# Kernel tuning notes

Measured on AMD Instinct MI355X. Metric: run time of the kernel, lower is better.

The kernel has to match this reference:

```python
import jax, jax.numpy as jnp
import numpy as np

N, E, D, H, K = 8192, 8, 1024, 4096, 2


def setup_inputs() -> dict:
    key = jax.random.key(0)
    ks = jax.random.split(key, 12)
    s = 0.02  # init scale for weights
    return {
        "x": jax.random.normal(ks[0], (N, D), jnp.float32),
        "noise": jax.random.normal(ks[1], (N, E), jnp.float32),
        "Wg_w": jax.random.normal(ks[2], (D, E), jnp.float32) * s,
        "Wg_b": jnp.zeros((E,), jnp.float32),
        "Wn_w": jax.random.normal(ks[3], (D, E), jnp.float32) * s,
        "Wn_b": jnp.zeros((E,), jnp.float32),
        "w1": jax.random.normal(ks[4], (E, D, H), jnp.float32) * s,
        "b1": jnp.zeros((E, H), jnp.float32),
        "w2": jax.random.normal(ks[5], (E, H, D), jnp.float32) * s,
        "b2": jnp.zeros((E, D), jnp.float32),
        "k": K,
    }


def reference(x, noise, Wg_w, Wg_b, Wn_w, Wn_b, w1, b1, w2, b2, k):
    # --- noisy top-k gating: H(x) = Wg(x) + noise * softplus(Wn(x)) ---
    g_logits = x @ Wg_w + Wg_b                       # [N, E]
    n_scale = jax.nn.softplus(x @ Wn_w + Wn_b)       # [N, E]
    h = g_logits + noise * n_scale                   # [N, E]
    topk_vals, topk_inds = jax.lax.top_k(h, k)       # [N, k]
    gates = jax.nn.softmax(topk_vals, axis=-1)       # [N, k]

    # Scatter top-k gates into a dense [N, E] map (zeros for unselected experts),
    # so the weighted combine is exactly sum_j gates[n,j] * expert_{inds[n,j]}(x_n).
    n_tok, n_exp = h.shape
    dense_gates = jnp.zeros((n_tok, n_exp), h.dtype).at[
        jnp.arange(n_tok)[:, None], topk_inds
    ].set(gates)                                     # [N, E]

    # --- per-expert 2-layer MLP: fc2(relu(fc1(x))) ---
    hid = jax.nn.relu(jnp.einsum('nd,edh->neh', x, w1) + b1)  # [N, E, H]
    y = jnp.einsum('neh,ehd->ned', hid, w2) + b2              # [N, E, D]
    out = jnp.einsum('ned,ne->nd', y, dense_gates)            # [N, D]
    return out
```

## Files before the change

### kernel.cpp

```cpp
#include <hip/hip_runtime.h>
#include <hip/hip_bf16.h>

#define NTOK 8192
#define NEXP 8
#define DMODEL 1024
#define DHID 4096

typedef __bf16 bf16x8 __attribute__((ext_vector_type(8)));
typedef float f32x4 __attribute__((ext_vector_type(4)));

__device__ __forceinline__ unsigned short f2bf(float f) {
  return __builtin_bit_cast(unsigned short, __float2bfloat16(f));
}

__device__ __forceinline__ void gload_lds16(const void* g, void* l) {
  __builtin_amdgcn_global_load_lds(
      (const __attribute__((address_space(1))) unsigned int*)g,
      (__attribute__((address_space(3))) unsigned int*)l, 16, 0, 0);
}

__device__ __forceinline__ int imin(int a, int b) { return a < b ? a : b; }

constexpr size_t OFF_XB   = 0;
constexpr size_t OFF_W1T  = OFF_XB + (size_t)NTOK * DMODEL * 2;
constexpr size_t OFF_W2T  = OFF_W1T + (size_t)NEXP * DHID * DMODEL * 2;
constexpr size_t OFF_HID  = OFF_W2T + (size_t)NEXP * DMODEL * DHID * 2;
constexpr size_t OFF_IDX  = OFF_HID + (size_t)NTOK * 2 * DHID * 2;
constexpr size_t OFF_GATE = OFF_IDX + (size_t)NTOK * 2 * 4;
constexpr size_t OFF_LIST = OFF_GATE + (size_t)NTOK * 2 * 4;
constexpr size_t OFF_CNT  = OFF_LIST + (size_t)NTOK * 2 * 4;
constexpr size_t OFF_OFFS = OFF_CNT + 128;
constexpr size_t OFF_CUR  = OFF_OFFS + 128;

__global__ void convert_x_kernel(const float4* __restrict__ in,
                                 ushort4* __restrict__ out, int n4) {
  int i = blockIdx.x * 256 + threadIdx.x;
  if (i < n4) {
    float4 v = in[i];
    ushort4 o;
    o.x = f2bf(v.x); o.y = f2bf(v.y); o.z = f2bf(v.z); o.w = f2bf(v.w);
    out[i] = o;
  }
}

__global__ void transpose_bf16_kernel(const float* __restrict__ in,
                                      unsigned short* __restrict__ out,
                                      int R, int C) {
  __shared__ float sh[32][33];
  const size_t ebase = (size_t)blockIdx.z * R * C;
  const float* ine = in + ebase;
  unsigned short* oute = out + ebase;
  int c0 = blockIdx.x * 32, r0 = blockIdx.y * 32;
  int tx = threadIdx.x & 31, ty = threadIdx.x >> 5;
#pragma unroll
  for (int i = 0; i < 4; ++i) {
    int r = ty + i * 8;
    sh[r][tx] = ine[(size_t)(r0 + r) * C + c0 + tx];
  }
  __syncthreads();
#pragma unroll
  for (int i = 0; i < 4; ++i) {
    int r = ty + i * 8;
    oute[(size_t)(c0 + r) * R + r0 + tx] = f2bf(sh[tx][r]);
  }
}

__global__ void gating_kernel(const float* __restrict__ x,
                              const float* __restrict__ noise,
                              const float* __restrict__ Wg_w,
                              const float* __restrict__ Wg_b,
                              const float* __restrict__ Wn_w,
                              const float* __restrict__ Wn_b,
                              int* __restrict__ topk_idx,
                              float* __restrict__ topk_gate,
                              int* __restrict__ counts) {
  int wave = threadIdx.x >> 6;
  int lane = threadIdx.x & 63;
  int n = blockIdx.x * 4 + wave;
  if (n >= NTOK) return;

  float ag[8] = {0.f, 0.f, 0.f, 0.f, 0.f, 0.f, 0.f, 0.f};
  float an[8] = {0.f, 0.f, 0.f, 0.f, 0.f, 0.f, 0.f, 0.f};
  const float* xr = x + (size_t)n * DMODEL;
#pragma unroll 4
  for (int i = 0; i < DMODEL / 64; ++i) {
    int d = lane + i * 64;
    float xv = xr[d];
    const float4* wg = (const float4*)(Wg_w + (size_t)d * 8);
    const float4* wn = (const float4*)(Wn_w + (size_t)d * 8);
    float4 g0 = wg[0], g1 = wg[1];
    float4 n0 = wn[0], n1 = wn[1];
    ag[0] += xv * g0.x; ag[1] += xv * g0.y; ag[2] += xv * g0.z; ag[3] += xv * g0.w;
    ag[4] += xv * g1.x; ag[5] += xv * g1.y; ag[6] += xv * g1.z; ag[7] += xv * g1.w;
    an[0] += xv * n0.x; an[1] += xv * n0.y; an[2] += xv * n0.z; an[3] += xv * n0.w;
    an[4] += xv * n1.x; an[5] += xv * n1.y; an[6] += xv * n1.z; an[7] += xv * n1.w;
  }
#pragma unroll
  for (int off = 32; off > 0; off >>= 1) {
#pragma unroll
    for (int j = 0; j < 8; ++j) {
      ag[j] += __shfl_down(ag[j], off, 64);
      an[j] += __shfl_down(an[j], off, 64);
    }
  }
  if (lane == 0) {
    float h[8];
#pragma unroll
    for (int e = 0; e < 8; ++e) {
      float gl = ag[e] + Wg_b[e];
      float z = an[e] + Wn_b[e];
      float sp = fmaxf(z, 0.f) + log1pf(expf(-fabsf(z)));
      h[e] = gl + noise[(size_t)n * 8 + e] * sp;
    }
    int i0 = 0; float v0 = h[0];
#pragma unroll
    for (int e = 1; e < 8; ++e)
      if (h[e] > v0) { v0 = h[e]; i0 = e; }
    int i1 = -1; float v1 = -1e30f;
#pragma unroll
    for (int e = 0; e < 8; ++e)
      if (e != i0 && h[e] > v1) { v1 = h[e]; i1 = e; }
    float e1 = expf(v1 - v0);
    float inv = 1.f / (1.f + e1);
    topk_idx[n * 2] = i0;
    topk_idx[n * 2 + 1] = i1;
    topk_gate[n * 2] = inv;
    topk_gate[n * 2 + 1] = e1 * inv;
    atomicAdd(&counts[i0], 1);
    atomicAdd(&counts[i1], 1);
  }
}

__global__ void scan_kernel(const int* __restrict__ counts,
                            int* __restrict__ offsets, int* __restrict__ cursor) {
  if (threadIdx.x == 0) {
    int acc = 0;
    for (int e = 0; e < NEXP; ++e) {
      offsets[e] = acc;
      cursor[e] = acc;
      acc += counts[e];
    }
    offsets[NEXP] = acc;
  }
}

__global__ void scatter_kernel(const int* __restrict__ topk_idx,
                               int* __restrict__ cursor, int* __restrict__ list) {
  int n = blockIdx.x * 256 + threadIdx.x;
  if (n >= NTOK) return;
#pragma unroll
  for (int j = 0; j < 2; ++j) {
    int e = topk_idx[n * 2 + j];
    int pos = atomicAdd(&cursor[e], 1);
    list[pos] = n * 2 + j;
  }
}

template <int MODE>
__global__ __launch_bounds__(256) void expert_gemm(
    const unsigned short* __restrict__ Asrc, const unsigned short* __restrict__ Bt,
    const float* __restrict__ bias, const int* __restrict__ offsets,
    const int* __restrict__ list, const float* __restrict__ gates,
    unsigned short* __restrict__ hid, float* __restrict__ out) {
  constexpr int K = MODE ? DHID : DMODEL;
  constexpr int Nout = MODE ? DMODEL : DHID;

  const int e = blockIdx.z;
  const int off = offsets[e];
  const int ne = offsets[e + 1] - off;
  const int m0 = blockIdx.y * 128;
  if (m0 >= ne) return;
  const int n0 = blockIdx.x * 128;

  __shared__ alignas(16) unsigned short Alds[128 * 32];
  __shared__ alignas(16) unsigned short Blds[128 * 32];

  const int tid = threadIdx.x;
  const int lane = tid & 63;
  const int w = tid >> 6;
  const int wm = (w >> 1) * 64;
  const int wn = (w & 1) * 64;
  const int lr = lane & 15;
  const int kg = lane >> 4;

  const unsigned short* srcA[2];
  const unsigned short* srcB[2];
#pragma unroll
  for (int i = 0; i < 2; ++i) {
    int q = tid + i * 256;
    int r = q >> 2, c = q & 3;
    int p = off + imin(m0 + r, ne - 1);
    if (MODE == 0) {
      int token = list[p] >> 1;
      srcA[i] = Asrc + (size_t)token * DMODEL + c * 8;
    } else {
      srcA[i] = Asrc + (size_t)p * DHID + c * 8;
    }
    srcB[i] = Bt + (size_t)e * Nout * K + (size_t)(n0 + r) * K + c * 8;
  }

  f32x4 acc[4][4] = {};

  for (int kt = 0; kt < K; kt += 32) {
#pragma unroll
    for (int i = 0; i < 2; ++i) {
      int q = tid + i * 256;
      gload_lds16(srcA[i] + kt, &Alds[q * 8]);
      gload_lds16(srcB[i] + kt, &Blds[q * 8]);
    }
    __syncthreads();

    bf16x8 af[4], bfr[4];
#pragma unroll
    for (int mf = 0; mf < 4; ++mf)
      af[mf] = *(const bf16x8*)&Alds[(wm + mf * 16 + lr) * 32 + kg * 8];
#pragma unroll
    for (int nf = 0; nf < 4; ++nf)
      bfr[nf] = *(const bf16x8*)&Blds[(wn + nf * 16 + lr) * 32 + kg * 8];
#pragma unroll
    for (int mf = 0; mf < 4; ++mf)
#pragma unroll
      for (int nf = 0; nf < 4; ++nf)
        acc[mf][nf] = __builtin_amdgcn_mfma_f32_16x16x32_bf16(af[mf], bfr[nf],
                                                              acc[mf][nf], 0, 0, 0);
    __syncthreads();
  }

  if (MODE == 0) {
#pragma unroll
    for (int mf = 0; mf < 4; ++mf) {
#pragma unroll
      for (int i = 0; i < 4; ++i) {
        int rloc = wm + mf * 16 + kg * 4 + i;
        int row = m0 + rloc;
        if (row < ne) {
          size_t p = (size_t)(off + row);
#pragma unroll
          for (int nf = 0; nf < 4; ++nf) {
            int col = n0 + wn + nf * 16 + lr;
            float v = acc[mf][nf][i] + bias[(size_t)e * Nout + col];
            v = fmaxf(v, 0.f);
            hid[p * DHID + col] = f2bf(v);
          }
        }
      }
    }
  } else {
#pragma unroll
    for (int mf = 0; mf < 4; ++mf) {
#pragma unroll
      for (int i = 0; i < 4; ++i) {
        int rloc = wm + mf * 16 + kg * 4 + i;
        int row = m0 + rloc;
        if (row < ne) {
          int lv = list[off + row];
          int token = lv >> 1;
          float g = gates[lv];
#pragma unroll
          for (int nf = 0; nf < 4; ++nf) {
            int col = n0 + wn + nf * 16 + lr;
            float v = (acc[mf][nf][i] + bias[(size_t)e * Nout + col]) * g;
            atomicAdd(&out[(size_t)token * DMODEL + col], v);
          }
        }
      }
    }
  }
}

extern "C" void kernel_launch(void* const* d_in, const int* in_sizes, int n_in,
                              void* d_out, int out_size, void* d_ws, size_t ws_size,
                              hipStream_t stream) {
  const float* x = (const float*)d_in[0];
  const float* noise = (const float*)d_in[1];
  const float* Wg_w = (const float*)d_in[2];
  const float* Wg_b = (const float*)d_in[3];
  const float* Wn_w = (const float*)d_in[4];
  const float* Wn_b = (const float*)d_in[5];
  const float* w1 = (const float*)d_in[6];
  const float* b1 = (const float*)d_in[7];
  const float* w2 = (const float*)d_in[8];
  const float* b2 = (const float*)d_in[9];
  float* out = (float*)d_out;

  char* ws = (char*)d_ws;
  unsigned short* xb = (unsigned short*)(ws + OFF_XB);
  unsigned short* w1t = (unsigned short*)(ws + OFF_W1T);
  unsigned short* w2t = (unsigned short*)(ws + OFF_W2T);
  unsigned short* hid = (unsigned short*)(ws + OFF_HID);
  int* topk_idx = (int*)(ws + OFF_IDX);
  float* topk_gate = (float*)(ws + OFF_GATE);
  int* list = (int*)(ws + OFF_LIST);
  int* counts = (int*)(ws + OFF_CNT);
  int* offsets = (int*)(ws + OFF_OFFS);
  int* cursor = (int*)(ws + OFF_CUR);

  hipMemsetAsync(out, 0, (size_t)NTOK * DMODEL * sizeof(float), stream);
  hipMemsetAsync(counts, 0, NEXP * sizeof(int), stream);

  {
    int n4 = NTOK * DMODEL / 4;
    convert_x_kernel<<<(n4 + 255) / 256, 256, 0, stream>>>((const float4*)x,
                                                           (ushort4*)xb, n4);
  }
  transpose_bf16_kernel<<<dim3(DHID / 32, DMODEL / 32, NEXP), 256, 0, stream>>>(
      w1, w1t, DMODEL, DHID);
  transpose_bf16_kernel<<<dim3(DMODEL / 32, DHID / 32, NEXP), 256, 0, stream>>>(
      w2, w2t, DHID, DMODEL);

  gating_kernel<<<NTOK / 4, 256, 0, stream>>>(x, noise, Wg_w, Wg_b, Wn_w, Wn_b,
                                              topk_idx, topk_gate, counts);
  scan_kernel<<<1, 64, 0, stream>>>(counts, offsets, cursor);
  scatter_kernel<<<NTOK / 256, 256, 0, stream>>>(topk_idx, cursor, list);

  expert_gemm<0><<<dim3(DHID / 128, NTOK / 128, NEXP), 256, 0, stream>>>(
      xb, w1t, b1, offsets, list, topk_gate, hid, nullptr);
  expert_gemm<1><<<dim3(DMODEL / 128, NTOK / 128, NEXP), 256, 0, stream>>>(
      hid, w2t, b2, offsets, list, topk_gate, nullptr, out);
}
```

Baseline: 888.4 us.

## Enlarge expert GEMM tiles to 256x256 with double-buffered swizzled LDS

The expert GEMM grows from 128x128 tiles with 4 waves to 256x256 tiles with 8 waves. It double-buffers the LDS stages so the next k-tile load overlaps the current MFMA work, XOR-swizzles the LDS columns to cut bank conflicts, and remaps block IDs so that adjacent workgroups spread across experts. The weight transpose also moves to 64x64 tiles with float4 loads and ushort4 stores. The aim is more data reuse and latency hiding per block, paid for with higher register and LDS pressure (64KB LDS, 128 accumulator floats per thread) and more wasted rows in the padded tail tiles per expert.

```diff
diff --git a/kernel.cpp b/kernel.cpp
--- a/kernel.cpp
+++ b/kernel.cpp
@@ -46,22 +46,31 @@
 __global__ void transpose_bf16_kernel(const float* __restrict__ in,
                                       unsigned short* __restrict__ out,
                                       int R, int C) {
-  __shared__ float sh[32][33];
+  __shared__ float sh[64][65];
   const size_t ebase = (size_t)blockIdx.z * R * C;
   const float* ine = in + ebase;
   unsigned short* oute = out + ebase;
-  int c0 = blockIdx.x * 32, r0 = blockIdx.y * 32;
-  int tx = threadIdx.x & 31, ty = threadIdx.x >> 5;
-#pragma unroll
-  for (int i = 0; i < 4; ++i) {
-    int r = ty + i * 8;
-    sh[r][tx] = ine[(size_t)(r0 + r) * C + c0 + tx];
+  int c0 = blockIdx.x * 64, r0 = blockIdx.y * 64;
+  int tx = threadIdx.x & 15, ty = threadIdx.x >> 4;
+#pragma unroll
+  for (int p = 0; p < 4; ++p) {
+    int row = ty + p * 16;
+    float4 v = *(const float4*)&ine[(size_t)(r0 + row) * C + c0 + tx * 4];
+    sh[row][tx * 4 + 0] = v.x;
+    sh[row][tx * 4 + 1] = v.y;
+    sh[row][tx * 4 + 2] = v.z;
+    sh[row][tx * 4 + 3] = v.w;
   }
   __syncthreads();
 #pragma unroll
-  for (int i = 0; i < 4; ++i) {
-    int r = ty + i * 8;
-    oute[(size_t)(c0 + r) * R + r0 + tx] = f2bf(sh[tx][r]);
+  for (int p = 0; p < 4; ++p) {
+    int crow = ty + p * 16;
+    ushort4 o;
+    o.x = f2bf(sh[tx * 4 + 0][crow]);
+    o.y = f2bf(sh[tx * 4 + 1][crow]);
+    o.z = f2bf(sh[tx * 4 + 2][crow]);
+    o.w = f2bf(sh[tx * 4 + 3][crow]);
+    *(ushort4*)&oute[(size_t)(c0 + crow) * R + r0 + tx * 4] = o;
   }
 }
 
@@ -157,100 +166,125 @@
 }
 
 template <int MODE>
-__global__ __launch_bounds__(256) void expert_gemm(
+__global__ __launch_bounds__(512, 2) void expert_gemm(
     const unsigned short* __restrict__ Asrc, const unsigned short* __restrict__ Bt,
     const float* __restrict__ bias, const int* __restrict__ offsets,
     const int* __restrict__ list, const float* __restrict__ gates,
     unsigned short* __restrict__ hid, float* __restrict__ out) {
   constexpr int K = MODE ? DHID : DMODEL;
   constexpr int Nout = MODE ? DMODEL : DHID;
-
-  const int e = blockIdx.z;
+  constexpr int NT = K / 32;
+
+  const int gx = gridDim.x, gy = gridDim.y;
+  const int nwg = gx * gy * NEXP;
+  const int lin = blockIdx.x + gx * (blockIdx.y + gy * blockIdx.z);
+  const int wg = (lin & 7) * (nwg >> 3) + (lin >> 3);
+  const int e = wg / (gx * gy);
+  const int t = wg % (gx * gy);
+  const int bx = t / gy;
+  const int by = t % gy;
+
   const int off = offsets[e];
   const int ne = offsets[e + 1] - off;
-  const int m0 = blockIdx.y * 128;
+  const int m0 = by * 256;
   if (m0 >= ne) return;
-  const int n0 = blockIdx.x * 128;
-
-  __shared__ alignas(16) unsigned short Alds[128 * 32];
-  __shared__ alignas(16) unsigned short Blds[128 * 32];
+  const int n0 = bx * 256;
+
+  __shared__ alignas(16) unsigned short Al[2][256 * 32];
+  __shared__ alignas(16) unsigned short Bl[2][256 * 32];
 
   const int tid = threadIdx.x;
   const int lane = tid & 63;
   const int w = tid >> 6;
-  const int wm = (w >> 1) * 64;
-  const int wn = (w & 1) * 64;
+  const int wMi = w >> 2;
+  const int wNi = w & 3;
   const int lr = lane & 15;
   const int kg = lane >> 4;
 
-  const unsigned short* srcA[2];
-  const unsigned short* srcB[2];
+  const unsigned short* a_src[2];
+  const unsigned short* b_src[2];
 #pragma unroll
   for (int i = 0; i < 2; ++i) {
-    int q = tid + i * 256;
-    int r = q >> 2, c = q & 3;
-    int p = off + imin(m0 + r, ne - 1);
+    int L = tid + i * 512;
+    int row = L >> 2, cc = L & 3;
+    int ccs = cc ^ ((row >> 1) & 3);
+    int p = off + imin(m0 + row, ne - 1);
     if (MODE == 0) {
       int token = list[p] >> 1;
-      srcA[i] = Asrc + (size_t)token * DMODEL + c * 8;
+      a_src[i] = Asrc + (size_t)token * DMODEL + ccs * 8;
     } else {
-      srcA[i] = Asrc + (size_t)p * DHID + c * 8;
-    }
-    srcB[i] = Bt + (size_t)e * Nout * K + (size_t)(n0 + r) * K + c * 8;
-  }
-
-  f32x4 acc[4][4] = {};
-
-  for (int kt = 0; kt < K; kt += 32) {
+      a_src[i] = Asrc + (size_t)p * DHID + ccs * 8;
+    }
+    b_src[i] = Bt + (size_t)e * Nout * K + (size_t)(n0 + row) * K + ccs * 8;
+  }
+
+  f32x4 acc[8][4] = {};
+
+  auto stage = [&](int buf, int kt) {
 #pragma unroll
     for (int i = 0; i < 2; ++i) {
-      int q = tid + i * 256;
-      gload_lds16(srcA[i] + kt, &Alds[q * 8]);
-      gload_lds16(srcB[i] + kt, &Blds[q * 8]);
-    }
+      gload_lds16(a_src[i] + kt * 32, &Al[buf][(tid + i * 512) * 8]);
+      gload_lds16(b_src[i] + kt * 32, &Bl[buf][(tid + i * 512) * 8]);
+    }
+  };
+
+  auto compute = [&](int buf) {
+    bf16x8 bfrag[4], afrag[8];
+#pragma unroll
+    for (int nf = 0; nf < 4; ++nf) {
+      int r = wNi * 64 + nf * 16 + lr;
+      int cc = kg ^ ((r >> 1) & 3);
+      bfrag[nf] = *(const bf16x8*)&Bl[buf][r * 32 + cc * 8];
+    }
+#pragma unroll
+    for (int mf = 0; mf < 8; ++mf) {
+      int r = wMi * 128 + mf * 16 + lr;
+      int cc = kg ^ ((r >> 1) & 3);
+      afrag[mf] = *(const bf16x8*)&Al[buf][r * 32 + cc * 8];
+    }
+#pragma unroll
+    for (int mf = 0; mf < 8; ++mf)
+#pragma unroll
+      for (int nf = 0; nf < 4; ++nf)
+        acc[mf][nf] = __builtin_amdgcn_mfma_f32_16x16x32_bf16(afrag[mf], bfrag[nf],
+                                                              acc[mf][nf], 0, 0, 0);
+  };
+
+  stage(0, 0);
+  __syncthreads();
+  int cur = 0;
+  for (int kt = 0; kt < NT - 1; ++kt) {
+    stage(cur ^ 1, kt + 1);
+    compute(cur);
     __syncthreads();
-
-    bf16x8 af[4], bfr[4];
-#pragma unroll
-    for (int mf = 0; mf < 4; ++mf)
-      af[mf] = *(const bf16x8*)&Alds[(wm + mf * 16 + lr) * 32 + kg * 8];
-#pragma unroll
-    for (int nf = 0; nf < 4; ++nf)
-      bfr[nf] = *(const bf16x8*)&Blds[(wn + nf * 16 + lr) * 32 + kg * 8];
-#pragma unroll
-    for (int mf = 0; mf < 4; ++mf)
-#pragma unroll
-      for (int nf = 0; nf < 4; ++nf)
-        acc[mf][nf] = __builtin_amdgcn_mfma_f32_16x16x32_bf16(af[mf], bfr[nf],
-                                                              acc[mf][nf], 0, 0, 0);
-    __syncthreads();
-  }
+    cur ^= 1;
+  }
+  compute(cur);
 
   if (MODE == 0) {
 #pragma unroll
-    for (int mf = 0; mf < 4; ++mf) {
-#pragma unroll
-      for (int i = 0; i < 4; ++i) {
-        int rloc = wm + mf * 16 + kg * 4 + i;
+    for (int mf = 0; mf < 8; ++mf) {
+#pragma unroll
+      for (int j = 0; j < 4; ++j) {
+        int rloc = wMi * 128 + mf * 16 + kg * 4 + j;
         int row = m0 + rloc;
         if (row < ne) {
           size_t p = (size_t)(off + row);
 #pragma unroll
           for (int nf = 0; nf < 4; ++nf) {
-            int col = n0 + wn + nf * 16 + lr;
-            float v = acc[mf][nf][i] + bias[(size_t)e * Nout + col];
-            v = fmaxf(v, 0.f);
-            hid[p * DHID + col] = f2bf(v);
+            int col = n0 + wNi * 64 + nf * 16 + lr;
+            float v = acc[mf][nf][j] + bias[(size_t)e * Nout + col];
+            hid[p * DHID + col] = f2bf(fmaxf(v, 0.f));
           }
         }
       }
     }
   } else {
 #pragma unroll
-    for (int mf = 0; mf < 4; ++mf) {
-#pragma unroll
-      for (int i = 0; i < 4; ++i) {
-        int rloc = wm + mf * 16 + kg * 4 + i;
+    for (int mf = 0; mf < 8; ++mf) {
+#pragma unroll
+      for (int j = 0; j < 4; ++j) {
+        int rloc = wMi * 128 + mf * 16 + kg * 4 + j;
         int row = m0 + rloc;
         if (row < ne) {
           int lv = list[off + row];
@@ -258,8 +292,8 @@
           float g = gates[lv];
 #pragma unroll
           for (int nf = 0; nf < 4; ++nf) {
-            int col = n0 + wn + nf * 16 + lr;
-            float v = (acc[mf][nf][i] + bias[(size_t)e * Nout + col]) * g;
+            int col = n0 + wNi * 64 + nf * 16 + lr;
+            float v = (acc[mf][nf][j] + bias[(size_t)e * Nout + col]) * g;
             atomicAdd(&out[(size_t)token * DMODEL + col], v);
           }
         }
@@ -303,9 +337,9 @@
     convert_x_kernel<<<(n4 + 255) / 256, 256, 0, stream>>>((const float4*)x,
                                                            (ushort4*)xb, n4);
   }
-  transpose_bf16_kernel<<<dim3(DHID / 32, DMODEL / 32, NEXP), 256, 0, stream>>>(
+  transpose_bf16_kernel<<<dim3(DHID / 64, DMODEL / 64, NEXP), 256, 0, stream>>>(
       w1, w1t, DMODEL, DHID);
-  transpose_bf16_kernel<<<dim3(DMODEL / 32, DHID / 32, NEXP), 256, 0, stream>>>(
+  transpose_bf16_kernel<<<dim3(DMODEL / 64, DHID / 64, NEXP), 256, 0, stream>>>(
       w2, w2t, DHID, DMODEL);
 
   gating_kernel<<<NTOK / 4, 256, 0, stream>>>(x, noise, Wg_w, Wg_b, Wn_w, Wn_b,
@@ -313,8 +347,8 @@
   scan_kernel<<<1, 64, 0, stream>>>(counts, offsets, cursor);
   scatter_kernel<<<NTOK / 256, 256, 0, stream>>>(topk_idx, cursor, list);
 
-  expert_gemm<0><<<dim3(DHID / 128, NTOK / 128, NEXP), 256, 0, stream>>>(
+  expert_gemm<0><<<dim3(DHID / 256, 32, NEXP), 512, 0, stream>>>(
       xb, w1t, b1, offsets, list, topk_gate, hid, nullptr);
-  expert_gemm<1><<<dim3(DMODEL / 128, NTOK / 128, NEXP), 256, 0, stream>>>(
+  expert_gemm<1><<<dim3(DMODEL / 256, 32, NEXP), 512, 0, stream>>>(
       hid, w2t, b2, offsets, list, topk_gate, nullptr, out);
 }
```

Result: slower. 1.162 ms (+30.8%).
